# Kernel tuning notes

Measured on AMD Instinct MI355X. Metric: run time of the kernel, lower is better.

Reference implementation:

```python
import jax, jax.numpy as jnp
import numpy as np

N_MODES = 64


def setup_inputs() -> dict:
    key = jax.random.key(0)
    k1, k2, k3 = jax.random.split(key, 3)
    B, Cin, S = 32, 128, 8192
    H, Hc, M = 4, 32, N_MODES  # n_heads, head_channels, n_modes (Cout = H*Hc = 128)
    x = jax.random.normal(k1, (B, Cin, S), dtype=jnp.float32)
    # per-head init scale: std = 0.01 * 2**h (matches _init_weights)
    scale = (0.01 * 2.0 ** jnp.arange(H, dtype=jnp.float32)).reshape(H, 1, 1, 1)
    w_real = jax.random.normal(k2, (H, Cin, Hc, M), dtype=jnp.float32) * scale
    w_imag = jax.random.normal(k3, (H, Cin, Hc, M), dtype=jnp.float32) * scale
    return {"x": x, "w_real": w_real, "w_imag": w_imag}


def reference(x, w_real, w_imag):
    B, Cin, S = x.shape
    H, _, Hc, M = w_real.shape
    Cout = H * Hc
    x_ft = jnp.fft.rfft(x, axis=-1)                 # [B, Cin, F] complex64
    F = x_ft.shape[-1]
    M = min(M, F)                                    # static
    w = (w_real + 1j * w_imag).astype(x_ft.dtype)    # [H, Cin, Hc, M]
    # fused batched complex contraction over all heads/modes at once
    out = jnp.einsum('bim,hiom->bhom', x_ft[:, :, :M], w[..., :M])  # [B, H, Hc, M]
    out = out.reshape(B, Cout, M)                    # head h -> channels [h*Hc, (h+1)*Hc)
    out_ft = jnp.zeros((B, Cout, F), dtype=x_ft.dtype).at[:, :, :M].set(out)
    return jnp.fft.irfft(out_ft, n=S, axis=-1)       # [B, Cout, S] float32
```

## Files before the change

kernel.cpp:

```cpp
#include <hip/hip_runtime.h>
#include <cstdio>

#define S_LEN 8192
#define NM 64

typedef short s8v __attribute__((ext_vector_type(8)));
typedef float f4  __attribute__((ext_vector_type(4)));
typedef _Float16 h8 __attribute__((ext_vector_type(8)));

static __device__ inline unsigned short f2bf(float f) {
    unsigned int u = __builtin_bit_cast(unsigned int, f);
    u = (u + 0x7FFFu + ((u >> 16) & 1u)) >> 16;
    return (unsigned short)u;
}
static __device__ inline float bf2f(unsigned short h) {
    unsigned int u = ((unsigned int)h) << 16;
    return __builtin_bit_cast(float, u);
}

#define SW32(r, k) (((r) * 32) + ((k) ^ ((((r) >> 1) & 3) << 3)))

static __device__ __forceinline__ void glds16(const void* g, void* l) {
    __builtin_amdgcn_global_load_lds(
        (const __attribute__((address_space(1))) unsigned int*)g,
        (__attribute__((address_space(3))) unsigned int*)l, 16, 0, 0);
}

__global__ __launch_bounds__(256) void gen_master(float* __restrict__ tab) {
    int p = blockIdx.x * 256 + threadIdx.x;
    tab[p] = cosf((float)p * (6.28318530717958647692f / (float)S_LEN));
}

__global__ __launch_bounds__(256) void gen_t1_img(const float* __restrict__ tab,
                                                  short* __restrict__ Th,
                                                  short* __restrict__ Tl) {
    int tid = blockIdx.x * 256 + threadIdx.x;
    int tile = tid >> 12;
    int sb = tile >> 2, kc = tile & 3;
    int us = tid & 4095;
    int ls = us >> 5, kx = us & 31;
    int lk = kx ^ (((ls >> 1) & 3) << 3);
    int s = sb * 128 + ls;
    int k = kc * 32 + lk;
    int m = k >> 1;
    int p = (m * s + ((k & 1) << 11)) & (S_LEN - 1);
    float v = tab[p];
    unsigned short h = f2bf(v);
    Th[tid] = (short)h;
    Tl[tid] = (short)f2bf(v - bf2f(h));
}

__global__ __launch_bounds__(256) void gen_b_img(const float* __restrict__ tab,
                                                 _Float16* __restrict__ Bimg) {
    int tid = blockIdx.x * 256 + threadIdx.x;
    int tk = tid >> 13;
    int us = tid & 8191;
    int c = us >> 6;
    int wl = us & 63;
    int slot = wl >> 3, e = wl & 7;
    int k = ((slot ^ (c & 7)) << 3) | e;
    int kg = tk * 64 + k;
    int m = c >> 1;
    int p = (m * kg + ((c & 1) << 11)) & (S_LEN - 1);
    Bimg[tid] = (_Float16)tab[p];
}

__global__ __launch_bounds__(512, 4) void dft_fwd_mfma(const float* __restrict__ x,
        const _Float16* __restrict__ Bimg, float* __restrict__ P) {
    __shared__ _Float16 abh[2][4096], abl[2][4096];
    __shared__ _Float16 bb[2][8192];
    const int t = threadIdx.x;
    const int lane = t & 63, w = t >> 6;
    const int rl = lane & 15, kq = lane >> 4;
    const int wr = w >> 2, wc = w & 3;
    const int row0 = blockIdx.x * 64;
    const int ks = blockIdx.y;
    const int rA = t >> 3, sA = t & 7;
    const size_t xrow = (size_t)(row0 + rA) * S_LEN + (size_t)ks * 1024 + (size_t)sA * 8;
    const int usA = rA * 64 + ((sA ^ (rA & 7)) << 3);
    const size_t bby = (size_t)ks * 16 * 16384 + (size_t)t * 32;

    f4 acc[2][2];
    #pragma unroll
    for (int i = 0; i < 2; ++i)
        #pragma unroll
        for (int j = 0; j < 2; ++j) acc[i][j] = (f4){0.f, 0.f, 0.f, 0.f};

    f4 aA0, aA1, aB0, aB1;
    h8 bA0, bA1, bB0, bB1;

    #define LA(SC, A0, A1) { A0 = *(const f4*)&x[xrow + (size_t)(SC) * 64];        \
                             A1 = *(const f4*)&x[xrow + (size_t)(SC) * 64 + 4]; }
    #define LB(SC, B0, B1) { const char* g = (const char*)Bimg + bby +             \
                                 (size_t)(SC) * 16384;                             \
                             B0 = *(const h8*)g; B1 = *(const h8*)(g + 16); }
    #define CV(A0, A1, NXT) { h8 hv, lv;                                           \
        _Pragma("unroll")                                                          \
        for (int e = 0; e < 4; ++e) {                                              \
            float f = A0[e]; _Float16 hh = (_Float16)f;                            \
            hv[e] = hh; lv[e] = (_Float16)(f - (float)hh);                         \
        }                                                                          \
        _Pragma("unroll")                                                          \
        for (int e = 0; e < 4; ++e) {                                              \
            float f = A1[e]; _Float16 hh = (_Float16)f;                            \
            hv[4 + e] = hh; lv[4 + e] = (_Float16)(f - (float)hh);                 \
        }                                                                          \
        *(h8*)&abh[NXT][usA] = hv;                                                 \
        *(h8*)&abl[NXT][usA] = lv; }
    #define WB(B0, B1, NXT) { *(h8*)&bb[NXT][t * 16] = B0;                         \
                              *(h8*)&bb[NXT][t * 16 + 8] = B1; }
    #define MM(CUR) { _Pragma("unroll")                                            \
        for (int ksl = 0; ksl < 2; ++ksl) {                                        \
            const int sb_ = ksl * 4 + kq;                                          \
            h8 Ah0, Al0, Ah1, Al1, Bv0, Bv1;                                       \
            { int r = wr * 32 + rl;      int u = r * 64 + ((sb_ ^ (r & 7)) << 3);  \
              Ah0 = *(const h8*)&abh[CUR][u]; Al0 = *(const h8*)&abl[CUR][u]; }    \
            { int r = wr * 32 + 16 + rl; int u = r * 64 + ((sb_ ^ (r & 7)) << 3);  \
              Ah1 = *(const h8*)&abh[CUR][u]; Al1 = *(const h8*)&abl[CUR][u]; }    \
            { int c = wc * 32 + rl;      int u = c * 64 + ((sb_ ^ (c & 7)) << 3);  \
              Bv0 = *(const h8*)&bb[CUR][u]; }                                     \
            { int c = wc * 32 + 16 + rl; int u = c * 64 + ((sb_ ^ (c & 7)) << 3);  \
              Bv1 = *(const h8*)&bb[CUR][u]; }                                     \
            acc[0][0] = __builtin_amdgcn_mfma_f32_16x16x32_f16(Ah0, Bv0, acc[0][0], 0, 0, 0); \
            acc[0][1] = __builtin_amdgcn_mfma_f32_16x16x32_f16(Ah0, Bv1, acc[0][1], 0, 0, 0); \
            acc[1][0] = __builtin_amdgcn_mfma_f32_16x16x32_f16(Ah1, Bv0, acc[1][0], 0, 0, 0); \
            acc[1][1] = __builtin_amdgcn_mfma_f32_16x16x32_f16(Ah1, Bv1, acc[1][1], 0, 0, 0); \
            acc[0][0] = __builtin_amdgcn_mfma_f32_16x16x32_f16(Al0, Bv0, acc[0][0], 0, 0, 0); \
            acc[0][1] = __builtin_amdgcn_mfma_f32_16x16x32_f16(Al0, Bv1, acc[0][1], 0, 0, 0); \
            acc[1][0] = __builtin_amdgcn_mfma_f32_16x16x32_f16(Al1, Bv0, acc[1][0], 0, 0, 0); \
            acc[1][1] = __builtin_amdgcn_mfma_f32_16x16x32_f16(Al1, Bv1, acc[1][1], 0, 0, 0); \
        } }
    #define BAR  __builtin_amdgcn_sched_barrier(0);                                \
        asm volatile("s_waitcnt lgkmcnt(0)" ::: "memory");                         \
        __builtin_amdgcn_sched_barrier(0);                                         \
        __builtin_amdgcn_s_barrier();                                              \
        __builtin_amdgcn_sched_barrier(0);

    LA(0, aA0, aA1) LA(1, aB0, aB1) LB(0, bA0, bA1) LB(1, bB0, bB1)
    __builtin_amdgcn_sched_barrier(0);
    CV(aA0, aA1, 0) WB(bA0, bA1, 0)
    BAR
    for (int s = 0; s < 14; s += 2) {
        LA(s + 2, aA0, aA1) LB(s + 2, bA0, bA1)
        __builtin_amdgcn_sched_barrier(0);
        CV(aB0, aB1, 1) WB(bB0, bB1, 1)
        MM(0)
        BAR
        LA(s + 3, aB0, aB1) LB(s + 3, bB0, bB1)
        __builtin_amdgcn_sched_barrier(0);
        CV(aA0, aA1, 0) WB(bA0, bA1, 0)
        MM(1)
        BAR
    }
    LA(15, aA0, aA1) LB(15, bA0, bA1)
    __builtin_amdgcn_sched_barrier(0);
    CV(aB0, aB1, 1) WB(bB0, bB1, 1)
    MM(0)
    BAR
    MM(1)

    float* Pks = P + (size_t)ks * 524288;
    #pragma unroll
    for (int mf = 0; mf < 2; ++mf)
        #pragma unroll
        for (int nf = 0; nf < 2; ++nf)
            #pragma unroll
            for (int r = 0; r < 4; ++r)
                Pks[(size_t)(row0 + wr * 32 + mf * 16 + kq * 4 + r) * 128
                    + wc * 32 + nf * 16 + rl] = acc[mf][nf][r];
}

__global__ __launch_bounds__(256) void ksum(const float* __restrict__ P,
                                            float* __restrict__ X) {
    int i = (blockIdx.x * 256 + threadIdx.x) * 4;
    f4 s = (f4){0.f, 0.f, 0.f, 0.f};
    #pragma unroll
    for (int ks = 0; ks < 8; ++ks)
        s += *(const f4*)&P[(size_t)ks * 524288 + i];
    *(f4*)&X[i] = s;
}

__global__ __launch_bounds__(256) void mode_contract(const float* __restrict__ X,
        const float* __restrict__ w_real, const float* __restrict__ w_imag,
        short* __restrict__ C2h, short* __restrict__ C2l) {
    __shared__ float xr[32][128], xi[32][128];
    __shared__ float wr[128][32], wi[128][32];
    const int m = blockIdx.x, h = blockIdx.y, t = threadIdx.x;
    #pragma unroll
    for (int it = 0; it < 16; ++it) {
        int li = t + it * 256;
        int b = li >> 7, i = li & 127;
        const float2 v = *(const float2*)&X[(size_t)(b * 128 + i) * 128 + 2 * m];
        xr[b][i] = v.x; xi[b][i] = v.y;
        int i2 = li >> 5, o = li & 31;
        size_t off = ((size_t)((h * 128 + i2) * 32 + o)) * NM + m;
        wr[i2][o] = w_real[off];
        wi[i2][o] = w_imag[off];
    }
    __syncthreads();
    const int o = t & 31;
    const int b0 = (t >> 5) * 4;
    float re[4] = {0.f, 0.f, 0.f, 0.f}, im[4] = {0.f, 0.f, 0.f, 0.f};
    for (int i = 0; i < 128; ++i) {
        float wrv = wr[i][o], wiv = wi[i][o];
        #pragma unroll
        for (int j = 0; j < 4; ++j) {
            float a = xr[b0 + j][i], c = xi[b0 + j][i];
            re[j] += a * wrv - c * wiv;
            im[j] += a * wiv + c * wrv;
        }
    }
    const float alpha = (m == 0) ? (1.0f / (float)S_LEN) : (2.0f / (float)S_LEN);
    const int kc = m >> 4;
    const int lk = (2 * m) & 31;
    #pragma unroll
    for (int j = 0; j < 4; ++j) {
        int row = (b0 + j) * 128 + h * 32 + o;
        float vr = alpha * re[j], vi = alpha * im[j];
        unsigned short hr = f2bf(vr), hi_ = f2bf(vi);
        float lr = vr - bf2f(hr), li_ = vi - bf2f(hi_);
        int rb = row >> 7, lr_ = row & 127;
        size_t ui = ((size_t)(rb * 4 + kc) * 4096 + SW32(lr_, lk)) >> 1;
        ((unsigned int*)C2h)[ui] = ((unsigned int)hi_ << 16) | hr;
        ((unsigned int*)C2l)[ui] = ((unsigned int)f2bf(li_) << 16) | f2bf(lr);
    }
}

__global__ __launch_bounds__(256, 2) void idft_mfma(const short* __restrict__ C2h,
        const short* __restrict__ C2l, const short* __restrict__ T1h,
        const short* __restrict__ T1l, float* __restrict__ y) {
    __shared__ short ah[2][4096], al[2][4096];
    __shared__ short bh[2][4096], bl[2][4096];
    const int t = threadIdx.x;
    const int lane = t & 63, wid = t >> 6;
    const int wm = (wid >> 1) * 64, wn = (wid & 1) * 64;
    const int sb = blockIdx.x;
    const int rb = blockIdx.y;
    f4 acc[4][4];
    #pragma unroll
    for (int i = 0; i < 4; ++i)
        #pragma unroll
        for (int j = 0; j < 4; ++j) acc[i][j] = (f4){0.f, 0.f, 0.f, 0.f};

    #define DMA3(kc, buf)  {                                                       \
        const size_t ta = (size_t)(rb * 4 + (kc)) * 8192;                          \
        const size_t tb = (size_t)(sb * 4 + (kc)) * 8192;                          \
        const int wo = wid * 2048 + lane * 16;                                     \
        glds16((const char*)C2h + ta + wo,        (char*)&ah[buf][0] + wid * 2048);        \
        glds16((const char*)C2h + ta + wo + 1024, (char*)&ah[buf][0] + wid * 2048 + 1024); \
        glds16((const char*)C2l + ta + wo,        (char*)&al[buf][0] + wid * 2048);        \
        glds16((const char*)C2l + ta + wo + 1024, (char*)&al[buf][0] + wid * 2048 + 1024); \
        glds16((const char*)T1h + tb + wo,        (char*)&bh[buf][0] + wid * 2048);        \
        glds16((const char*)T1h + tb + wo + 1024, (char*)&bh[buf][0] + wid * 2048 + 1024); \
        glds16((const char*)T1l + tb + wo,        (char*)&bl[buf][0] + wid * 2048);        \
        glds16((const char*)T1l + tb + wo + 1024, (char*)&bl[buf][0] + wid * 2048 + 1024); }

    DMA3(0, 0);
    __syncthreads();
    #pragma unroll
    for (int kc = 0; kc < 4; ++kc) {
        const int cur = kc & 1;
        if (kc < 3) DMA3(kc + 1, cur ^ 1);
        {
            const int kk = (lane >> 4) * 8, rl = lane & 15;
            s8v Ah[4], Al[4], Bh[4], Bl[4];
            #pragma unroll
            for (int mf = 0; mf < 4; ++mf) {
                int us = SW32(wm + mf * 16 + rl, kk);
                Ah[mf] = *(const s8v*)&ah[cur][us];
                Al[mf] = *(const s8v*)&al[cur][us];
            }
            #pragma unroll
            for (int nf = 0; nf < 4; ++nf) {
                int us = SW32(wn + nf * 16 + rl, kk);
                Bh[nf] = *(const s8v*)&bh[cur][us];
                Bl[nf] = *(const s8v*)&bl[cur][us];
            }
            #pragma unroll
            for (int mf = 0; mf < 4; ++mf)
                #pragma unroll
                for (int nf = 0; nf < 4; ++nf)
                    acc[mf][nf] = __builtin_amdgcn_mfma_f32_16x16x32_bf16(Ah[mf], Bh[nf], acc[mf][nf], 0, 0, 0);
            #pragma unroll
            for (int mf = 0; mf < 4; ++mf)
                #pragma unroll
                for (int nf = 0; nf < 4; ++nf)
                    acc[mf][nf] = __builtin_amdgcn_mfma_f32_16x16x32_bf16(Al[mf], Bh[nf], acc[mf][nf], 0, 0, 0);
            #pragma unroll
            for (int mf = 0; mf < 4; ++mf)
                #pragma unroll
                for (int nf = 0; nf < 4; ++nf)
                    acc[mf][nf] = __builtin_amdgcn_mfma_f32_16x16x32_bf16(Ah[mf], Bl[nf], acc[mf][nf], 0, 0, 0);
        }
        __syncthreads();
    }
    #pragma unroll
    for (int mf = 0; mf < 4; ++mf) {
        int rr = rb * 128 + wm + mf * 16 + (lane >> 4) * 4;
        #pragma unroll
        for (int nf = 0; nf < 4; ++nf) {
            int c = sb * 128 + wn + nf * 16 + (lane & 15);
            #pragma unroll
            for (int r = 0; r < 4; ++r)
                __builtin_nontemporal_store(acc[mf][nf][r], &y[(size_t)(rr + r) * S_LEN + c]);
        }
    }
}

extern "C" void kernel_launch(void* const* d_in, const int* in_sizes, int n_in,
                              void* d_out, int out_size, void* d_ws, size_t ws_size,
                              hipStream_t stream) {
    const float* x      = (const float*)d_in[0];
    const float* w_real = (const float*)d_in[1];
    const float* w_imag = (const float*)d_in[2];
    float* y = (float*)d_out;

    const size_t TBL = (size_t)S_LEN * 128;
    char* w0 = (char*)d_ws;
    short* T1h     = (short*)w0;
    short* T1l     = T1h + TBL;
    _Float16* Bimg = (_Float16*)(T1l + TBL);
    float* X       = (float*)(Bimg + TBL);
    float* tab     = X + (size_t)4096 * 128;
    float* P       = tab + S_LEN;
    short* C2h     = (short*)P;
    short* C2l     = C2h + TBL;
    const size_t TOTAL = (size_t)((char*)(P + 8 * (size_t)4096 * 128) - w0);
    if (ws_size < TOTAL) {
        fprintf(stderr, "kernel_launch: ws too small (%zu < %zu bytes)\n", ws_size, TOTAL);
        return;
    }

    gen_master<<<S_LEN / 256, 256, 0, stream>>>(tab);
    gen_t1_img<<<(S_LEN * 128) / 256, 256, 0, stream>>>(tab, T1h, T1l);
    gen_b_img<<<(S_LEN * 128) / 256, 256, 0, stream>>>(tab, Bimg);
    dft_fwd_mfma<<<dim3(64, 8), 512, 0, stream>>>(x, Bimg, P);
    ksum<<<512, 256, 0, stream>>>(P, X);
    mode_contract<<<dim3(NM, 4), 256, 0, stream>>>(X, w_real, w_imag, C2h, C2l);
    idft_mfma<<<dim3(S_LEN / 128, 4096 / 128), 256, 0, stream>>>(C2h, C2l, T1h, T1l, y);
}
```

Measured before the change: 123.3 us.

## Fuse split-K reduction into mode contraction, deepen forward pipeline, stream idft twiddles from global

The separate ksum kernel is removed and mode_contract now sums the eight split-K partials itself as it loads them, saving a launch and a round trip through an intermediate buffer. The forward DFT loop moves from a 2-deep to a 3-deep register prefetch of x and is fully unrolled. The inverse DFT now stages all four coefficient tiles in LDS once up front and reads the twiddle table straight from global memory into registers in an unswizzled layout, instead of double-buffering both operands through LDS with barriers. The trade-off is more uncoalesced loads in mode_contract, more global/L2 traffic for the twiddles in idft, and extra register pressure.

```diff
diff --git a/kernel.cpp b/kernel.cpp
--- a/kernel.cpp
+++ b/kernel.cpp
@@ -31,23 +31,22 @@
     tab[p] = cosf((float)p * (6.28318530717958647692f / (float)S_LEN));
 }
 
-__global__ __launch_bounds__(256) void gen_t1_img(const float* __restrict__ tab,
-                                                  short* __restrict__ Th,
-                                                  short* __restrict__ Tl) {
-    int tid = blockIdx.x * 256 + threadIdx.x;
-    int tile = tid >> 12;
+__global__ __launch_bounds__(256) void gen_t1f(const float* __restrict__ tab,
+                                               short* __restrict__ Th,
+                                               short* __restrict__ Tl) {
+    int u = blockIdx.x * 256 + threadIdx.x;
+    int tile = u >> 12;
     int sb = tile >> 2, kc = tile & 3;
-    int us = tid & 4095;
-    int ls = us >> 5, kx = us & 31;
-    int lk = kx ^ (((ls >> 1) & 3) << 3);
-    int s = sb * 128 + ls;
-    int k = kc * 32 + lk;
+    int uw = u & 4095;
+    int c = uw >> 5, rest = uw & 31;
+    int k = kc * 32 + rest;
+    int s = sb * 128 + c;
     int m = k >> 1;
     int p = (m * s + ((k & 1) << 11)) & (S_LEN - 1);
     float v = tab[p];
     unsigned short h = f2bf(v);
-    Th[tid] = (short)h;
-    Tl[tid] = (short)f2bf(v - bf2f(h));
+    Th[u] = (short)h;
+    Tl[u] = (short)f2bf(v - bf2f(h));
 }
 
 __global__ __launch_bounds__(256) void gen_b_img(const float* __restrict__ tab,
@@ -86,15 +85,15 @@
         #pragma unroll
         for (int j = 0; j < 2; ++j) acc[i][j] = (f4){0.f, 0.f, 0.f, 0.f};
 
-    f4 aA0, aA1, aB0, aB1;
-    h8 bA0, bA1, bB0, bB1;
-
-    #define LA(SC, A0, A1) { A0 = *(const f4*)&x[xrow + (size_t)(SC) * 64];        \
-                             A1 = *(const f4*)&x[xrow + (size_t)(SC) * 64 + 4]; }
-    #define LB(SC, B0, B1) { const char* g = (const char*)Bimg + bby +             \
-                                 (size_t)(SC) * 16384;                             \
-                             B0 = *(const h8*)g; B1 = *(const h8*)(g + 16); }
-    #define CV(A0, A1, NXT) { h8 hv, lv;                                           \
+    f4 aP[3][2];
+    h8 bP[2][2];
+
+    #define LA_(SC, A0, A1) { A0 = *(const f4*)&x[xrow + (size_t)(SC) * 64];       \
+                              A1 = *(const f4*)&x[xrow + (size_t)(SC) * 64 + 4]; }
+    #define LB_(SC, B0, B1) { const char* g = (const char*)Bimg + bby +            \
+                                  (size_t)(SC) * 16384;                            \
+                              B0 = *(const h8*)g; B1 = *(const h8*)(g + 16); }
+    #define CV_(A0, A1, NXT) { h8 hv, lv;                                          \
         _Pragma("unroll")                                                          \
         for (int e = 0; e < 4; ++e) {                                              \
             float f = A0[e]; _Float16 hh = (_Float16)f;                            \
@@ -107,9 +106,9 @@
         }                                                                          \
         *(h8*)&abh[NXT][usA] = hv;                                                 \
         *(h8*)&abl[NXT][usA] = lv; }
-    #define WB(B0, B1, NXT) { *(h8*)&bb[NXT][t * 16] = B0;                         \
-                              *(h8*)&bb[NXT][t * 16 + 8] = B1; }
-    #define MM(CUR) { _Pragma("unroll")                                            \
+    #define WB_(B0, B1, NXT) { *(h8*)&bb[NXT][t * 16] = B0;                        \
+                               *(h8*)&bb[NXT][t * 16 + 8] = B1; }
+    #define MM_(CUR) { _Pragma("unroll")                                           \
         for (int ksl = 0; ksl < 2; ++ksl) {                                        \
             const int sb_ = ksl * 4 + kq;                                          \
             h8 Ah0, Al0, Ah1, Al1, Bv0, Bv1;                                       \
@@ -130,34 +129,31 @@
             acc[1][0] = __builtin_amdgcn_mfma_f32_16x16x32_f16(Al1, Bv0, acc[1][0], 0, 0, 0); \
             acc[1][1] = __builtin_amdgcn_mfma_f32_16x16x32_f16(Al1, Bv1, acc[1][1], 0, 0, 0); \
         } }
-    #define BAR  __builtin_amdgcn_sched_barrier(0);                                \
+    #define BAR_ __builtin_amdgcn_sched_barrier(0);                                \
         asm volatile("s_waitcnt lgkmcnt(0)" ::: "memory");                         \
         __builtin_amdgcn_sched_barrier(0);                                         \
         __builtin_amdgcn_s_barrier();                                              \
         __builtin_amdgcn_sched_barrier(0);
 
-    LA(0, aA0, aA1) LA(1, aB0, aB1) LB(0, bA0, bA1) LB(1, bB0, bB1)
-    __builtin_amdgcn_sched_barrier(0);
-    CV(aA0, aA1, 0) WB(bA0, bA1, 0)
-    BAR
-    for (int s = 0; s < 14; s += 2) {
-        LA(s + 2, aA0, aA1) LB(s + 2, bA0, bA1)
+    {
+        f4 t0a, t0b; h8 tb0a, tb0b;
+        LA_(0, t0a, t0b) LB_(0, tb0a, tb0b)
+        LA_(1, aP[1][0], aP[1][1]) LA_(2, aP[2][0], aP[2][1])
+        LB_(1, bP[1][0], bP[1][1])
         __builtin_amdgcn_sched_barrier(0);
-        CV(aB0, aB1, 1) WB(bB0, bB1, 1)
-        MM(0)
-        BAR
-        LA(s + 3, aB0, aB1) LB(s + 3, bB0, bB1)
+        CV_(t0a, t0b, 0) WB_(tb0a, tb0b, 0)
+        BAR_
+    }
+    #pragma unroll
+    for (int s = 0; s < 16; ++s) {
+        if (s + 3 <= 15) LA_(s + 3, aP[(s + 3) % 3][0], aP[(s + 3) % 3][1])
+        if (s + 2 <= 15) LB_(s + 2, bP[(s + 2) & 1][0], bP[(s + 2) & 1][1])
         __builtin_amdgcn_sched_barrier(0);
-        CV(aA0, aA1, 0) WB(bA0, bA1, 0)
-        MM(1)
-        BAR
-    }
-    LA(15, aA0, aA1) LB(15, bA0, bA1)
-    __builtin_amdgcn_sched_barrier(0);
-    CV(aB0, aB1, 1) WB(bB0, bB1, 1)
-    MM(0)
-    BAR
-    MM(1)
+        if (s + 1 <= 15) { CV_(aP[(s + 1) % 3][0], aP[(s + 1) % 3][1], (s + 1) & 1)
+                           WB_(bP[(s + 1) & 1][0], bP[(s + 1) & 1][1], (s + 1) & 1) }
+        MM_(s & 1)
+        if (s < 15) { BAR_ }
+    }
 
     float* Pks = P + (size_t)ks * 524288;
     #pragma unroll
@@ -170,17 +166,7 @@
                     + wc * 32 + nf * 16 + rl] = acc[mf][nf][r];
 }
 
-__global__ __launch_bounds__(256) void ksum(const float* __restrict__ P,
-                                            float* __restrict__ X) {
-    int i = (blockIdx.x * 256 + threadIdx.x) * 4;
-    f4 s = (f4){0.f, 0.f, 0.f, 0.f};
-    #pragma unroll
-    for (int ks = 0; ks < 8; ++ks)
-        s += *(const f4*)&P[(size_t)ks * 524288 + i];
-    *(f4*)&X[i] = s;
-}
-
-__global__ __launch_bounds__(256) void mode_contract(const float* __restrict__ X,
+__global__ __launch_bounds__(256) void mode_contract(const float* __restrict__ P,
         const float* __restrict__ w_real, const float* __restrict__ w_imag,
         short* __restrict__ C2h, short* __restrict__ C2l) {
     __shared__ float xr[32][128], xi[32][128];
@@ -190,8 +176,14 @@
     for (int it = 0; it < 16; ++it) {
         int li = t + it * 256;
         int b = li >> 7, i = li & 127;
-        const float2 v = *(const float2*)&X[(size_t)(b * 128 + i) * 128 + 2 * m];
-        xr[b][i] = v.x; xi[b][i] = v.y;
+        float re = 0.f, im = 0.f;
+        #pragma unroll
+        for (int ks = 0; ks < 8; ++ks) {
+            const float2 v = *(const float2*)&P[(size_t)ks * 524288
+                                                + (size_t)(b * 128 + i) * 128 + 2 * m];
+            re += v.x; im += v.y;
+        }
+        xr[b][i] = re; xi[b][i] = im;
         int i2 = li >> 5, o = li & 31;
         size_t off = ((size_t)((h * 128 + i2) * 32 + o)) * NM + m;
         wr[i2][o] = w_real[off];
@@ -227,79 +219,73 @@
 }
 
 __global__ __launch_bounds__(256, 2) void idft_mfma(const short* __restrict__ C2h,
-        const short* __restrict__ C2l, const short* __restrict__ T1h,
-        const short* __restrict__ T1l, float* __restrict__ y) {
-    __shared__ short ah[2][4096], al[2][4096];
-    __shared__ short bh[2][4096], bl[2][4096];
+        const short* __restrict__ C2l, const short* __restrict__ T1fH,
+        const short* __restrict__ T1fL, float* __restrict__ y) {
+    __shared__ short ah[4][4096], al[4][4096];
     const int t = threadIdx.x;
-    const int lane = t & 63, wid = t >> 6;
-    const int wm = (wid >> 1) * 64, wn = (wid & 1) * 64;
-    const int sb = blockIdx.x;
-    const int rb = blockIdx.y;
+    const int lane = t & 63, w = t >> 6;
+    const int rl = lane & 15, kq = lane >> 4;
+    const int wm = (w >> 1) * 64, wn = (w & 1) * 64;
+    const int sb = blockIdx.x, rb = blockIdx.y;
+
+    #pragma unroll
+    for (int kc = 0; kc < 4; ++kc) {
+        const size_t ta = (size_t)(rb * 4 + kc) * 8192;
+        const int wo = w * 2048 + lane * 16;
+        glds16((const char*)C2h + ta + wo,        (char*)&ah[kc][0] + w * 2048);
+        glds16((const char*)C2h + ta + wo + 1024, (char*)&ah[kc][0] + w * 2048 + 1024);
+        glds16((const char*)C2l + ta + wo,        (char*)&al[kc][0] + w * 2048);
+        glds16((const char*)C2l + ta + wo + 1024, (char*)&al[kc][0] + w * 2048 + 1024);
+    }
+    __syncthreads();
+
     f4 acc[4][4];
     #pragma unroll
     for (int i = 0; i < 4; ++i)
         #pragma unroll
         for (int j = 0; j < 4; ++j) acc[i][j] = (f4){0.f, 0.f, 0.f, 0.f};
 
-    #define DMA3(kc, buf)  {                                                       \
-        const size_t ta = (size_t)(rb * 4 + (kc)) * 8192;                          \
-        const size_t tb = (size_t)(sb * 4 + (kc)) * 8192;                          \
-        const int wo = wid * 2048 + lane * 16;                                     \
-        glds16((const char*)C2h + ta + wo,        (char*)&ah[buf][0] + wid * 2048);        \
-        glds16((const char*)C2h + ta + wo + 1024, (char*)&ah[buf][0] + wid * 2048 + 1024); \
-        glds16((const char*)C2l + ta + wo,        (char*)&al[buf][0] + wid * 2048);        \
-        glds16((const char*)C2l + ta + wo + 1024, (char*)&al[buf][0] + wid * 2048 + 1024); \
-        glds16((const char*)T1h + tb + wo,        (char*)&bh[buf][0] + wid * 2048);        \
-        glds16((const char*)T1h + tb + wo + 1024, (char*)&bh[buf][0] + wid * 2048 + 1024); \
-        glds16((const char*)T1l + tb + wo,        (char*)&bl[buf][0] + wid * 2048);        \
-        glds16((const char*)T1l + tb + wo + 1024, (char*)&bl[buf][0] + wid * 2048 + 1024); }
-
-    DMA3(0, 0);
-    __syncthreads();
     #pragma unroll
     for (int kc = 0; kc < 4; ++kc) {
-        const int cur = kc & 1;
-        if (kc < 3) DMA3(kc + 1, cur ^ 1);
-        {
-            const int kk = (lane >> 4) * 8, rl = lane & 15;
-            s8v Ah[4], Al[4], Bh[4], Bl[4];
-            #pragma unroll
-            for (int mf = 0; mf < 4; ++mf) {
-                int us = SW32(wm + mf * 16 + rl, kk);
-                Ah[mf] = *(const s8v*)&ah[cur][us];
-                Al[mf] = *(const s8v*)&al[cur][us];
-            }
-            #pragma unroll
-            for (int nf = 0; nf < 4; ++nf) {
-                int us = SW32(wn + nf * 16 + rl, kk);
-                Bh[nf] = *(const s8v*)&bh[cur][us];
-                Bl[nf] = *(const s8v*)&bl[cur][us];
-            }
-            #pragma unroll
-            for (int mf = 0; mf < 4; ++mf)
-                #pragma unroll
-                for (int nf = 0; nf < 4; ++nf)
-                    acc[mf][nf] = __builtin_amdgcn_mfma_f32_16x16x32_bf16(Ah[mf], Bh[nf], acc[mf][nf], 0, 0, 0);
-            #pragma unroll
-            for (int mf = 0; mf < 4; ++mf)
-                #pragma unroll
-                for (int nf = 0; nf < 4; ++nf)
-                    acc[mf][nf] = __builtin_amdgcn_mfma_f32_16x16x32_bf16(Al[mf], Bh[nf], acc[mf][nf], 0, 0, 0);
-            #pragma unroll
-            for (int mf = 0; mf < 4; ++mf)
-                #pragma unroll
-                for (int nf = 0; nf < 4; ++nf)
-                    acc[mf][nf] = __builtin_amdgcn_mfma_f32_16x16x32_bf16(Ah[mf], Bl[nf], acc[mf][nf], 0, 0, 0);
-        }
-        __syncthreads();
-    }
+        s8v Bh[4], Bl[4];
+        const size_t tb = (size_t)(sb * 4 + kc) * 8192 + (size_t)rl * 64 + (size_t)kq * 16;
+        #pragma unroll
+        for (int nf = 0; nf < 4; ++nf) {
+            const size_t off = tb + (size_t)(wn + nf * 16) * 64;
+            Bh[nf] = *(const s8v*)((const char*)T1fH + off);
+            Bl[nf] = *(const s8v*)((const char*)T1fL + off);
+        }
+        const int kk = kq * 8;
+        s8v Ah[4], Al[4];
+        #pragma unroll
+        for (int mf = 0; mf < 4; ++mf) {
+            int us = SW32(wm + mf * 16 + rl, kk);
+            Ah[mf] = *(const s8v*)&ah[kc][us];
+            Al[mf] = *(const s8v*)&al[kc][us];
+        }
+        #pragma unroll
+        for (int mf = 0; mf < 4; ++mf)
+            #pragma unroll
+            for (int nf = 0; nf < 4; ++nf)
+                acc[mf][nf] = __builtin_amdgcn_mfma_f32_16x16x32_bf16(Ah[mf], Bh[nf], acc[mf][nf], 0, 0, 0);
+        #pragma unroll
+        for (int mf = 0; mf < 4; ++mf)
+            #pragma unroll
+            for (int nf = 0; nf < 4; ++nf)
+                acc[mf][nf] = __builtin_amdgcn_mfma_f32_16x16x32_bf16(Al[mf], Bh[nf], acc[mf][nf], 0, 0, 0);
+        #pragma unroll
+        for (int mf = 0; mf < 4; ++mf)
+            #pragma unroll
+            for (int nf = 0; nf < 4; ++nf)
+                acc[mf][nf] = __builtin_amdgcn_mfma_f32_16x16x32_bf16(Ah[mf], Bl[nf], acc[mf][nf], 0, 0, 0);
+    }
+
     #pragma unroll
     for (int mf = 0; mf < 4; ++mf) {
-        int rr = rb * 128 + wm + mf * 16 + (lane >> 4) * 4;
+        int rr = rb * 128 + wm + mf * 16 + kq * 4;
         #pragma unroll
         for (int nf = 0; nf < 4; ++nf) {
-            int c = sb * 128 + wn + nf * 16 + (lane & 15);
+            int c = sb * 128 + wn + nf * 16 + rl;
             #pragma unroll
             for (int r = 0; r < 4; ++r)
                 __builtin_nontemporal_store(acc[mf][nf][r], &y[(size_t)(rr + r) * S_LEN + c]);
@@ -317,14 +303,13 @@
 
     const size_t TBL = (size_t)S_LEN * 128;
     char* w0 = (char*)d_ws;
-    short* T1h     = (short*)w0;
-    short* T1l     = T1h + TBL;
-    _Float16* Bimg = (_Float16*)(T1l + TBL);
-    float* X       = (float*)(Bimg + TBL);
-    float* tab     = X + (size_t)4096 * 128;
-    float* P       = tab + S_LEN;
-    short* C2h     = (short*)P;
+    short* T1fH    = (short*)w0;
+    short* T1fL    = T1fH + TBL;
+    _Float16* Bimg = (_Float16*)(T1fL + TBL);
+    float* tab     = (float*)(Bimg + TBL);
+    short* C2h     = (short*)(tab + S_LEN);
     short* C2l     = C2h + TBL;
+    float* P       = (float*)(C2l + TBL);
     const size_t TOTAL = (size_t)((char*)(P + 8 * (size_t)4096 * 128) - w0);
     if (ws_size < TOTAL) {
         fprintf(stderr, "kernel_launch: ws too small (%zu < %zu bytes)\n", ws_size, TOTAL);
@@ -332,10 +317,9 @@
     }
 
     gen_master<<<S_LEN / 256, 256, 0, stream>>>(tab);
-    gen_t1_img<<<(S_LEN * 128) / 256, 256, 0, stream>>>(tab, T1h, T1l);
+    gen_t1f<<<(S_LEN * 128) / 256, 256, 0, stream>>>(tab, T1fH, T1fL);
     gen_b_img<<<(S_LEN * 128) / 256, 256, 0, stream>>>(tab, Bimg);
     dft_fwd_mfma<<<dim3(64, 8), 512, 0, stream>>>(x, Bimg, P);
-    ksum<<<512, 256, 0, stream>>>(P, X);
-    mode_contract<<<dim3(NM, 4), 256, 0, stream>>>(X, w_real, w_imag, C2h, C2l);
-    idft_mfma<<<dim3(S_LEN / 128, 4096 / 128), 256, 0, stream>>>(C2h, C2l, T1h, T1l, y);
-}
+    mode_contract<<<dim3(NM, 4), 256, 0, stream>>>(P, w_real, w_imag, C2h, C2l);
+    idft_mfma<<<dim3(64, 32), 256, 0, stream>>>(C2h, C2l, T1fH, T1fL, y);
+}
```

Result: slower. 155.4 us (+26.0%).
